# Performance work log

Measured on AMD Instinct MI355X. Metric: run time of the kernel, lower is better.

The kernel has to match this reference:

```python
import jax, jax.numpy as jnp
import numpy as np

B, N, DIM = 4, 2048, 128
K = 32            # num_nearest_neighbors
FF = 4            # fourier_features
M_DIM = 16
EDGE_IN = FF * 2 + DIM * 2 + 1  # 265


def setup_inputs() -> dict:
    key = jax.random.key(0)
    ks = jax.random.split(key, 16)
    std = 0.001  # init_eps normal init for Linear weights
    p = {
        "feats": jax.random.normal(ks[0], (B, N, DIM), jnp.float32),
        "coors": jax.random.normal(ks[1], (B, N, 3), jnp.float32),
        # edge_mlp: Linear(265, 530) -> SiLU -> Linear(530, 16) -> SiLU
        "eW1": jax.random.normal(ks[2], (EDGE_IN, EDGE_IN * 2), jnp.float32) * std,
        "eb1": jax.random.normal(ks[3], (EDGE_IN * 2,), jnp.float32) * std,
        "eW2": jax.random.normal(ks[4], (EDGE_IN * 2, M_DIM), jnp.float32) * std,
        "eb2": jax.random.normal(ks[5], (M_DIM,), jnp.float32) * std,
        # coors_mlp: Linear(16, 64) -> SiLU -> Linear(64, 1)
        "cW1": jax.random.normal(ks[6], (M_DIM, M_DIM * 4), jnp.float32) * std,
        "cb1": jax.random.normal(ks[7], (M_DIM * 4,), jnp.float32) * std,
        "cW2": jax.random.normal(ks[8], (M_DIM * 4, 1), jnp.float32) * std,
        "cb2": jax.random.normal(ks[9], (1,), jnp.float32) * std,
        # node_mlp: Linear(144, 256) -> SiLU -> Linear(256, 128)
        "nW1": jax.random.normal(ks[10], (DIM + M_DIM, DIM * 2), jnp.float32) * std,
        "nb1": jax.random.normal(ks[11], (DIM * 2,), jnp.float32) * std,
        "nW2": jax.random.normal(ks[12], (DIM * 2, DIM), jnp.float32) * std,
        "nb2": jax.random.normal(ks[13], (DIM,), jnp.float32) * std,
    }
    return p


def _egnn_fwd(feats, coors, eW1, eb1, eW2, eb2, cW1, cb1, cW2, cb2, nW1, nb1, nW2, nb2):
    # all-pairs squared distances: [b, n, n]
    rel_coors_full = coors[:, :, None, :] - coors[:, None, :, :]
    rel_dist = jnp.sum(rel_coors_full * rel_coors_full, axis=-1)

    # top-k nearest (smallest distance) -> indices [b, n, k]
    _, idx = jax.lax.top_k(-rel_dist, K)

    # gather neighbor coords / feats per batch: [b, n, k, *]
    coors_j = jax.vmap(lambda x, i: x[i])(coors, idx)
    feats_j = jax.vmap(lambda x, i: x[i])(feats, idx)
    rel_coors = coors[:, :, None, :] - coors_j                     # b n k 3
    d = jnp.take_along_axis(rel_dist, idx, axis=2)[..., None]       # b n k 1

    # fourier encode distances: [b, n, k, 2*FF + 1]
    scales = 2.0 ** jnp.arange(FF, dtype=feats.dtype)               # [FF]
    xs = d[..., None] / scales                                      # b n k 1 FF
    enc = jnp.concatenate([jnp.sin(xs), jnp.cos(xs), d[..., None]], axis=-1)
    enc = enc[..., 0, :]                                            # b n k (2FF+1)

    feats_i = jnp.broadcast_to(feats[:, :, None, :], feats_j.shape)
    edge_input = jnp.concatenate([feats_i, feats_j, enc], axis=-1)  # b n k 265

    # edge MLP -> messages m_ij [b, n, k, m_dim]
    h = jax.nn.silu(edge_input @ eW1 + eb1)
    m_ij = jax.nn.silu(h @ eW2 + eb2)

    # coors MLP -> per-edge coordinate weights [b, n, k]
    cw = (jax.nn.silu(m_ij @ cW1 + cb1) @ cW2 + cb2)[..., 0]
    coors_out = jnp.einsum('bij,bijc->bic', cw, rel_coors) + coors

    # node update: sum-pool messages, concat with feats, MLP + residual
    m_i = jnp.sum(m_ij, axis=-2)                                    # b n m_dim
    node_in = jnp.concatenate([feats, m_i], axis=-1)
    node_out = jax.nn.silu(node_in @ nW1 + nb1) @ nW2 + nb2 + feats
    return node_out, coors_out


def reference(feats, coors, eW1, eb1, eW2, eb2, cW1, cb1, cW2, cb2, nW1, nb1, nW2, nb2):
    return _egnn_fwd(feats, coors, eW1, eb1, eW2, eb2, cW1, cb1, cW2, cb2, nW1, nb1, nW2, nb2)
```

## Files before the change

### kernel.cpp

```cpp
#include <hip/hip_runtime.h>
#include <hip/hip_bf16.h>
#include <math.h>

#define Bb 4
#define Nn 2048
#define DIMd 128
#define Kk 32
#define H1 530
#define PW2 530
#define MD 16
#define NDH 256
#define NDI 144

typedef float f32x2 __attribute__((ext_vector_type(2)));
typedef float f32x4 __attribute__((ext_vector_type(4)));
typedef short s16x4 __attribute__((ext_vector_type(4)));
typedef short s16x8 __attribute__((ext_vector_type(8)));

__device__ __forceinline__ unsigned short f2bf(float f){
    union { float f; unsigned u; } v; v.f = f;
    unsigned r = v.u + 0x7FFFu + ((v.u >> 16) & 1u);
    return (unsigned short)(r >> 16);
}
__device__ __forceinline__ float silu_f(float x){
    float e = __builtin_amdgcn_exp2f(x * -1.442695041f);
    return x * __builtin_amdgcn_rcpf(1.0f + e);
}
__device__ __forceinline__ f32x2 silu2(f32x2 x){
    float e0 = __builtin_amdgcn_exp2f(x[0] * -1.442695041f);
    float e1 = __builtin_amdgcn_exp2f(x[1] * -1.442695041f);
    f32x2 r;
    r[0] = x[0] * __builtin_amdgcn_rcpf(1.0f + e0);
    r[1] = x[1] * __builtin_amdgcn_rcpf(1.0f + e1);
    return r;
}
__device__ __forceinline__ unsigned cvt_pk_bf16(float a, float b){
    unsigned r;
    asm("v_cvt_pk_bf16_f32 %0, %1, %2" : "=v"(r) : "v"(a), "v"(b));
    return r;
}

__global__ __launch_bounds__(256) void topk_kernel(const float* __restrict__ coors,
        int* __restrict__ idx_ws, float* __restrict__ dv_ws){
    int tid = threadIdx.x;
    int w = tid >> 6, lane = tid & 63;
    int node = blockIdx.x * 4 + w;
    int b = node >> 11;
    const float* cbp = coors + (size_t)b * Nn * 3;
    float cx = coors[node*3+0], cy = coors[node*3+1], cz = coors[node*3+2];
    float d[32];
    #pragma unroll
    for (int t = 0; t < 32; t++){
        int j = t*64 + lane;
        float dx = cx - cbp[j*3+0], dy = cy - cbp[j*3+1], dz = cz - cbp[j*3+2];
        d[t] = dx*dx + dy*dy + dz*dz;
    }
    float md = d[0]; int mj = lane;
    #pragma unroll
    for (int t = 1; t < 32; t++){
        int jt = t*64 + lane;
        if (d[t] < md){ md = d[t]; mj = jt; }
    }
    for (int r = 0; r < Kk; r++){
        float bd = md; int bj = mj;
        #pragma unroll
        for (int off = 32; off; off >>= 1){
            float d2 = __shfl_xor(bd, off); int j2 = __shfl_xor(bj, off);
            if (d2 < bd || (d2 == bd && j2 < bj)){ bd = d2; bj = j2; }
        }
        if (lane == 0){
            idx_ws[node*Kk + r] = bj;
            dv_ws[node*Kk + r] = bd;
        }
        if (mj == bj){
            md = 3.4e38f; mj = 0x7fffffff;
            #pragma unroll
            for (int t = 0; t < 32; t++){
                int jt = t*64 + lane;
                if (jt == bj) d[t] = 3.4e38f;
                if (d[t] < md){ md = d[t]; mj = jt; }
            }
        }
    }
}

__global__ __launch_bounds__(256) void fragw_kernel(const float* __restrict__ eW1,
        const float* __restrict__ eW2,
        unsigned short* __restrict__ W1F, unsigned short* __restrict__ WPF,
        unsigned short* __restrict__ W2F2){
    int i0 = blockIdx.x * 256 + threadIdx.x;
    int stride = gridDim.x * 256;
    for (int i = i0; i < 34*5*512; i += stride){
        int j = i & 7, lane = (i >> 3) & 63, t = i >> 9;
        int ks = t % 5, nt = t / 5;
        int cg = nt*16 + (lane & 15);
        int k = ks*32 + ((lane >> 4) << 3) + j;
        float v = 0.f;
        if (cg < H1){
            if (k < 128) v = eW1[(size_t)(128+k)*H1 + cg];
            else if (k < 137) v = eW1[(size_t)(256+(k-128))*H1 + cg];
        }
        W1F[i] = f2bf(v);
    }
    for (int i = i0; i < 34*4*512; i += stride){
        int j = i & 7, lane = (i >> 3) & 63, t = i >> 9;
        int ks = t & 3, nt = t >> 2;
        int cg = nt*16 + (lane & 15);
        int k = ks*32 + ((lane >> 4) << 3) + j;
        float v = (cg < H1) ? eW1[(size_t)k*H1 + cg] : 0.f;
        WPF[i] = f2bf(v);
    }
    for (int i = i0; i < 34*512; i += stride){
        int j = i & 7, lane = (i >> 3) & 63, nt = i >> 9;
        int kl = ((lane >> 4) << 3) + j;
        int col = lane & 15;
        int row = nt*16 + kl;
        float v = (kl < 16 && row < H1) ? eW2[(size_t)row*MD + col] : 0.f;
        W2F2[i] = f2bf(v);
    }
}

__global__ __launch_bounds__(256) void pmat_kernel(const float* __restrict__ feats,
        const unsigned short* __restrict__ WPF, const float* __restrict__ eb1,
        float* __restrict__ P){
    int tid = threadIdx.x;
    int wid = tid >> 6, lane = tid & 63;
    int node0 = blockIdx.x * 32;
    int kg = (lane >> 4) * 8;
    s16x8 af[2][4];
    #pragma unroll
    for (int m = 0; m < 2; m++){
        const float* fr = feats + (size_t)(node0 + m*16 + (lane & 15)) * DIMd;
        #pragma unroll
        for (int ks = 0; ks < 4; ks++){
            f32x4 lo = *(const f32x4*)(fr + ks*32 + kg);
            f32x4 hi = *(const f32x4*)(fr + ks*32 + kg + 4);
            union { s16x8 v; unsigned u[4]; } pk;
            pk.u[0] = cvt_pk_bf16(lo[0], lo[1]); pk.u[1] = cvt_pk_bf16(lo[2], lo[3]);
            pk.u[2] = cvt_pk_bf16(hi[0], hi[1]); pk.u[3] = cvt_pk_bf16(hi[2], hi[3]);
            af[m][ks] = pk.v;
        }
    }
    const s16x8* WPFv = (const s16x8*)WPF;
    for (int nt = wid; nt < 34; nt += 4){
        f32x4 acc0 = {0,0,0,0}, acc1 = {0,0,0,0};
        #pragma unroll
        for (int ks = 0; ks < 4; ks++){
            s16x8 bb = WPFv[(nt*4 + ks)*64 + lane];
            acc0 = __builtin_amdgcn_mfma_f32_16x16x32_bf16(af[0][ks], bb, acc0, 0, 0, 0);
            acc1 = __builtin_amdgcn_mfma_f32_16x16x32_bf16(af[1][ks], bb, acc1, 0, 0, 0);
        }
        int cg = nt*16 + (lane & 15);
        if (cg < H1){
            float b = eb1[cg];
            int r0 = (lane >> 4) * 4;
            #pragma unroll
            for (int r = 0; r < 4; r++){
                P[(size_t)(node0 + r0 + r)*PW2 + cg]      = acc0[r] + b;
                P[(size_t)(node0 + 16 + r0 + r)*PW2 + cg] = acc1[r] + b;
            }
        }
    }
}

#define TS 24
__global__ __launch_bounds__(256, 5) void edge_kernel(const float* __restrict__ coors,
        const float* __restrict__ feats, const float* __restrict__ eb2,
        const float* __restrict__ cW1, const float* __restrict__ cb1,
        const float* __restrict__ cW2, const float* __restrict__ cb2,
        const float* __restrict__ P, const unsigned short* __restrict__ W1F,
        const unsigned short* __restrict__ W2F2,
        const int* __restrict__ idx_ws, const float* __restrict__ dv_ws,
        float* __restrict__ mi_ws, float* __restrict__ coors_out){
    __shared__ float Pi_lds[544];
    __shared__ __align__(16) unsigned short aenc[Kk][32];
    __shared__ int js[Kk];
    __shared__ float rels[Kk][3];
    __shared__ unsigned short T[4][16][TS];
    __shared__ float m_red[4][Kk][MD];
    __shared__ float cacc[4][3];

    int node = blockIdx.x; int tid = threadIdx.x;
    int b = node >> 11;
    int wid = tid >> 6, lane = tid & 63;

    for (int t = tid; t < 4*16*(TS-16); t += 256){
        int w = t / (16*(TS-16)), rem = t % (16*(TS-16));
        T[w][rem / (TS-16)][16 + rem % (TS-16)] = 0;
    }
    const float* Pn = P + (size_t)node*PW2;
    Pi_lds[tid]       = Pn[tid];
    { int c = tid + 256; Pi_lds[c] = (c < PW2) ? Pn[c] : 0.f; }
    if (tid < 32){ int c = 512 + tid; Pi_lds[c] = (c < PW2) ? Pn[c] : 0.f; }
    if (tid < Kk){
        int j = idx_ws[node*Kk + tid];
        float dv = dv_ws[node*Kk + tid];
        js[tid] = j;
        unsigned short e[9];
        e[0] = f2bf(sinf(dv));        e[1] = f2bf(sinf(dv*0.5f));
        e[2] = f2bf(sinf(dv*0.25f));  e[3] = f2bf(sinf(dv*0.125f));
        e[4] = f2bf(cosf(dv));        e[5] = f2bf(cosf(dv*0.5f));
        e[6] = f2bf(cosf(dv*0.25f));  e[7] = f2bf(cosf(dv*0.125f));
        e[8] = f2bf(dv);
        #pragma unroll
        for (int q = 0; q < 9; q++) aenc[tid][q] = e[q];
        #pragma unroll
        for (int q = 9; q < 32; q++) aenc[tid][q] = 0;
        int jg = (b << 11) + j;
        rels[tid][0] = coors[node*3+0] - coors[jg*3+0];
        rels[tid][1] = coors[node*3+1] - coors[jg*3+1];
        rels[tid][2] = coors[node*3+2] - coors[jg*3+2];
    }
    __syncthreads();

    int kg = (lane >> 4) * 8;
    int kga = (kg >= 16) ? 16 : kg;
    s16x8 af[2][5];
    #pragma unroll
    for (int m = 0; m < 2; m++){
        int row = m*16 + (lane & 15);
        int jgl = (b << 11) + js[row];
        const float* fr = feats + (size_t)jgl * DIMd;
        #pragma unroll
        for (int ks = 0; ks < 4; ks++){
            f32x4 lo = *(const f32x4*)(fr + ks*32 + kg);
            f32x4 hi = *(const f32x4*)(fr + ks*32 + kg + 4);
            union { s16x8 v; unsigned u[4]; } pk;
            pk.u[0] = cvt_pk_bf16(lo[0], lo[1]); pk.u[1] = cvt_pk_bf16(lo[2], lo[3]);
            pk.u[2] = cvt_pk_bf16(hi[0], hi[1]); pk.u[3] = cvt_pk_bf16(hi[2], hi[3]);
            af[m][ks] = pk.v;
        }
        af[m][4] = *(const s16x8*)(&aenc[row][kg]);
    }

    const s16x8* W1Fv  = (const s16x8*)W1F;
    const s16x8* W2F2v = (const s16x8*)W2F2;
    f32x4 macc0 = {0,0,0,0}, macc1 = {0,0,0,0};
    int col = lane & 15, r0 = (lane >> 4) * 4;
    for (int nt = wid; nt < 34; nt += 4){
        f32x4 acc0 = {0,0,0,0}, acc1 = {0,0,0,0};
        #pragma unroll
        for (int ks = 0; ks < 5; ks++){
            s16x8 bb = W1Fv[(nt*5 + ks)*64 + lane];
            acc0 = __builtin_amdgcn_mfma_f32_16x16x32_bf16(af[0][ks], bb, acc0, 0, 0, 0);
            acc1 = __builtin_amdgcn_mfma_f32_16x16x32_bf16(af[1][ks], bb, acc1, 0, 0, 0);
        }
        int cg = nt*16 + col;
        bool valid = cg < H1;
        float pic = Pi_lds[cg];
        s16x8 w2b = W2F2v[nt*64 + lane];
        #pragma unroll
        for (int r = 0; r < 4; r++)
            T[wid][r0 + r][col] = valid ? f2bf(silu_f(acc0[r] + pic)) : (unsigned short)0;
        {
            union { s16x8 v; s16x4 h[2]; } a2;
            a2.h[0] = *(const s16x4*)&T[wid][col][kga];
            a2.h[1] = *(const s16x4*)&T[wid][col][kga + 4];
            macc0 = __builtin_amdgcn_mfma_f32_16x16x32_bf16(a2.v, w2b, macc0, 0, 0, 0);
        }
        #pragma unroll
        for (int r = 0; r < 4; r++)
            T[wid][r0 + r][col] = valid ? f2bf(silu_f(acc1[r] + pic)) : (unsigned short)0;
        {
            union { s16x8 v; s16x4 h[2]; } a2;
            a2.h[0] = *(const s16x4*)&T[wid][col][kga];
            a2.h[1] = *(const s16x4*)&T[wid][col][kga + 4];
            macc1 = __builtin_amdgcn_mfma_f32_16x16x32_bf16(a2.v, w2b, macc1, 0, 0, 0);
        }
    }
    #pragma unroll
    for (int r = 0; r < 4; r++){
        m_red[wid][r0 + r][col]      = macc0[r];
        m_red[wid][16 + r0 + r][col] = macc1[r];
    }
    __syncthreads();
    #pragma unroll
    for (int t = tid; t < Kk*MD; t += 256){
        int n = t >> 4, f = t & 15;
        float s = m_red[0][n][f] + m_red[1][n][f] + m_red[2][n][f] + m_red[3][n][f];
        m_red[0][n][f] = silu_f(s + eb2[f]);
    }
    __syncthreads();
    if (tid < MD){
        float s = 0.f;
        #pragma unroll
        for (int n = 0; n < Kk; n++) s += m_red[0][n][tid];
        mi_ws[node*MD + tid] = s;
    }
    float vx = 0.f, vy = 0.f, vz = 0.f;
    int u4 = col * 4;
    f32x4 cb14 = *(const f32x4*)(cb1 + u4);
    f32x4 c24  = *(const f32x4*)(cW2 + u4);
    #pragma unroll
    for (int q = 0; q < 2; q++){
        int eid = wid*8 + (lane >> 4)*2 + q;
        f32x4 acc4 = cb14;
        #pragma unroll
        for (int f = 0; f < MD; f++){
            float mv = m_red[0][eid][f];
            f32x4 w4 = *(const f32x4*)(cW1 + f*64 + u4);
            acc4 += (f32x4){mv,mv,mv,mv} * w4;
        }
        float p = silu_f(acc4[0])*c24[0] + silu_f(acc4[1])*c24[1]
                + silu_f(acc4[2])*c24[2] + silu_f(acc4[3])*c24[3];
        #pragma unroll
        for (int off = 1; off < 16; off <<= 1) p += __shfl_xor(p, off);
        float cw = p + cb2[0];
        if (col == 0){
            vx += cw * rels[eid][0];
            vy += cw * rels[eid][1];
            vz += cw * rels[eid][2];
        }
    }
    vx += __shfl_xor(vx, 16); vx += __shfl_xor(vx, 32);
    vy += __shfl_xor(vy, 16); vy += __shfl_xor(vy, 32);
    vz += __shfl_xor(vz, 16); vz += __shfl_xor(vz, 32);
    if (lane == 0){ cacc[wid][0] = vx; cacc[wid][1] = vy; cacc[wid][2] = vz; }
    __syncthreads();
    if (tid == 0){
        coors_out[node*3+0] = cacc[0][0]+cacc[1][0]+cacc[2][0]+cacc[3][0] + coors[node*3+0];
        coors_out[node*3+1] = cacc[0][1]+cacc[1][1]+cacc[2][1]+cacc[3][1] + coors[node*3+1];
        coors_out[node*3+2] = cacc[0][2]+cacc[1][2]+cacc[2][2]+cacc[3][2] + coors[node*3+2];
    }
}

__global__ __launch_bounds__(256) void node_kernel(const float* __restrict__ feats,
        const float* __restrict__ mi_ws,
        const float* __restrict__ nW1, const float* __restrict__ nb1,
        const float* __restrict__ nW2, const float* __restrict__ nb2,
        float* __restrict__ out){
    __shared__ float insT[NDI][12];
    __shared__ float hsdT[NDH][12];
    int tid = threadIdx.x;
    int node0 = blockIdx.x * 8;
    for (int t = tid; t < 8*DIMd; t += 256){
        int m = t >> 7, k = t & 127;
        insT[k][m] = feats[(size_t)node0*DIMd + t];
    }
    if (tid < 8*MD) insT[DIMd + (tid & 15)][tid >> 4] = mi_ws[node0*MD + tid];
    __syncthreads();
    float bias = nb1[tid];
    f32x2 acc[4];
    #pragma unroll
    for (int p = 0; p < 4; p++) acc[p] = (f32x2){bias, bias};
    for (int k = 0; k < NDI; k++){
        float wv = nW1[(size_t)k*NDH + tid];
        f32x2 w2 = {wv, wv};
        acc[0] += *(const f32x2*)&insT[k][0] * w2;
        acc[1] += *(const f32x2*)&insT[k][2] * w2;
        acc[2] += *(const f32x2*)&insT[k][4] * w2;
        acc[3] += *(const f32x2*)&insT[k][6] * w2;
    }
    #pragma unroll
    for (int p = 0; p < 4; p++) *(f32x2*)&hsdT[tid][2*p] = silu2(acc[p]);
    __syncthreads();
    int c = tid & 127, half = tid >> 7;
    float b2 = nb2[c];
    f32x2 a0 = {b2, b2}, a1 = {b2, b2};
    for (int k = 0; k < NDH; k++){
        float wv = nW2[(size_t)k*DIMd + c];
        f32x2 w2 = {wv, wv};
        a0 += *(const f32x2*)&hsdT[k][half*4]     * w2;
        a1 += *(const f32x2*)&hsdT[k][half*4 + 2] * w2;
    }
    #pragma unroll
    for (int q = 0; q < 4; q++){
        int m = half*4 + q;
        float v = (q < 2) ? a0[q & 1] : a1[q & 1];
        out[(size_t)(node0+m)*DIMd + c] = v + feats[(size_t)(node0+m)*DIMd + c];
    }
}

extern "C" void kernel_launch(void* const* d_in, const int* in_sizes, int n_in,
                              void* d_out, int out_size, void* d_ws, size_t ws_size,
                              hipStream_t stream){
    const float* feats = (const float*)d_in[0];
    const float* coors = (const float*)d_in[1];
    const float* eW1 = (const float*)d_in[2];
    const float* eb1 = (const float*)d_in[3];
    const float* eW2 = (const float*)d_in[4];
    const float* eb2 = (const float*)d_in[5];
    const float* cW1 = (const float*)d_in[6];
    const float* cb1 = (const float*)d_in[7];
    const float* cW2 = (const float*)d_in[8];
    const float* cb2 = (const float*)d_in[9];
    const float* nW1 = (const float*)d_in[10];
    const float* nb1 = (const float*)d_in[11];
    const float* nW2 = (const float*)d_in[12];
    const float* nb2 = (const float*)d_in[13];
    float* out = (float*)d_out;
    float* coors_out = out + (size_t)Bb*Nn*DIMd;

    char* ws = (char*)d_ws;
    size_t off = 0;
    int*   idx_ws = (int*)(ws + off);   off += (1u<<20);
    float* dv_ws  = (float*)(ws + off); off += (1u<<20);
    float* Pd     = (float*)(ws + off); off += 17367040u;
    float* mi_ws  = (float*)(ws + off); off += 524288u;
    unsigned short* W1F  = (unsigned short*)(ws + off); off += 174080u;
    unsigned short* WPF  = (unsigned short*)(ws + off); off += 139264u;
    unsigned short* W2F2 = (unsigned short*)(ws + off); off += 34816u;

    fragw_kernel<<<256, 256, 0, stream>>>(eW1, eW2, W1F, WPF, W2F2);
    pmat_kernel<<<Bb*Nn/32, 256, 0, stream>>>(feats, WPF, eb1, Pd);
    topk_kernel<<<Bb*Nn/4, 256, 0, stream>>>(coors, idx_ws, dv_ws);
    edge_kernel<<<Bb*Nn, 256, 0, stream>>>(coors, feats, eb2, cW1, cb1, cW2, cb2,
                                           Pd, W1F, W2F2, idx_ws, dv_ws, mi_ws, coors_out);
    node_kernel<<<Bb*Nn/8, 256, 0, stream>>>(feats, mi_ws, nW1, nb1, nW2, nb2, out);
}
```

Baseline: 304.9 us.

## Merge topk and pmat kernels; transpose edge MFMAs, pass hidden via bpermute

Merges the top-k and P-matrix kernels into one launch that branches on block index, so both independent stages can run concurrently and one launch is saved. In the edge kernel it swaps the MFMA operand order, putting weights in the A operand and edge features in B. The silu'd hidden tile then stays in registers and is redistributed with ds_bpermute for the second MFMA, replacing the per-wave LDS transpose buffer and its zero-fill. It also pads m_red against bank conflicts and raises the occupancy hint from 5 to 8 waves, which risks register spills.

```diff
diff --git a/kernel.cpp b/kernel.cpp
--- a/kernel.cpp
+++ b/kernel.cpp
@@ -11,10 +11,11 @@
 #define MD 16
 #define NDH 256
 #define NDI 144
+#define TOPK_BLKS (Bb*Nn/4)
+#define PMAT_BLKS (Bb*Nn/32)
 
 typedef float f32x2 __attribute__((ext_vector_type(2)));
 typedef float f32x4 __attribute__((ext_vector_type(4)));
-typedef short s16x4 __attribute__((ext_vector_type(4)));
 typedef short s16x8 __attribute__((ext_vector_type(8)));
 
 __device__ __forceinline__ unsigned short f2bf(float f){
@@ -38,50 +39,6 @@
     unsigned r;
     asm("v_cvt_pk_bf16_f32 %0, %1, %2" : "=v"(r) : "v"(a), "v"(b));
     return r;
-}
-
-__global__ __launch_bounds__(256) void topk_kernel(const float* __restrict__ coors,
-        int* __restrict__ idx_ws, float* __restrict__ dv_ws){
-    int tid = threadIdx.x;
-    int w = tid >> 6, lane = tid & 63;
-    int node = blockIdx.x * 4 + w;
-    int b = node >> 11;
-    const float* cbp = coors + (size_t)b * Nn * 3;
-    float cx = coors[node*3+0], cy = coors[node*3+1], cz = coors[node*3+2];
-    float d[32];
-    #pragma unroll
-    for (int t = 0; t < 32; t++){
-        int j = t*64 + lane;
-        float dx = cx - cbp[j*3+0], dy = cy - cbp[j*3+1], dz = cz - cbp[j*3+2];
-        d[t] = dx*dx + dy*dy + dz*dz;
-    }
-    float md = d[0]; int mj = lane;
-    #pragma unroll
-    for (int t = 1; t < 32; t++){
-        int jt = t*64 + lane;
-        if (d[t] < md){ md = d[t]; mj = jt; }
-    }
-    for (int r = 0; r < Kk; r++){
-        float bd = md; int bj = mj;
-        #pragma unroll
-        for (int off = 32; off; off >>= 1){
-            float d2 = __shfl_xor(bd, off); int j2 = __shfl_xor(bj, off);
-            if (d2 < bd || (d2 == bd && j2 < bj)){ bd = d2; bj = j2; }
-        }
-        if (lane == 0){
-            idx_ws[node*Kk + r] = bj;
-            dv_ws[node*Kk + r] = bd;
-        }
-        if (mj == bj){
-            md = 3.4e38f; mj = 0x7fffffff;
-            #pragma unroll
-            for (int t = 0; t < 32; t++){
-                int jt = t*64 + lane;
-                if (jt == bj) d[t] = 3.4e38f;
-                if (d[t] < md){ md = d[t]; mj = jt; }
-            }
-        }
-    }
 }
 
 __global__ __launch_bounds__(256) void fragw_kernel(const float* __restrict__ eW1,
@@ -120,51 +77,94 @@
     }
 }
 
-__global__ __launch_bounds__(256) void pmat_kernel(const float* __restrict__ feats,
+__global__ __launch_bounds__(256) void prep_kernel(const float* __restrict__ coors,
+        const float* __restrict__ feats,
         const unsigned short* __restrict__ WPF, const float* __restrict__ eb1,
-        float* __restrict__ P){
+        int* __restrict__ idx_ws, float* __restrict__ dv_ws, float* __restrict__ P){
+    int bid = blockIdx.x;
     int tid = threadIdx.x;
-    int wid = tid >> 6, lane = tid & 63;
-    int node0 = blockIdx.x * 32;
-    int kg = (lane >> 4) * 8;
-    s16x8 af[2][4];
-    #pragma unroll
-    for (int m = 0; m < 2; m++){
-        const float* fr = feats + (size_t)(node0 + m*16 + (lane & 15)) * DIMd;
-        #pragma unroll
-        for (int ks = 0; ks < 4; ks++){
-            f32x4 lo = *(const f32x4*)(fr + ks*32 + kg);
-            f32x4 hi = *(const f32x4*)(fr + ks*32 + kg + 4);
-            union { s16x8 v; unsigned u[4]; } pk;
-            pk.u[0] = cvt_pk_bf16(lo[0], lo[1]); pk.u[1] = cvt_pk_bf16(lo[2], lo[3]);
-            pk.u[2] = cvt_pk_bf16(hi[0], hi[1]); pk.u[3] = cvt_pk_bf16(hi[2], hi[3]);
-            af[m][ks] = pk.v;
-        }
-    }
-    const s16x8* WPFv = (const s16x8*)WPF;
-    for (int nt = wid; nt < 34; nt += 4){
-        f32x4 acc0 = {0,0,0,0}, acc1 = {0,0,0,0};
-        #pragma unroll
-        for (int ks = 0; ks < 4; ks++){
-            s16x8 bb = WPFv[(nt*4 + ks)*64 + lane];
-            acc0 = __builtin_amdgcn_mfma_f32_16x16x32_bf16(af[0][ks], bb, acc0, 0, 0, 0);
-            acc1 = __builtin_amdgcn_mfma_f32_16x16x32_bf16(af[1][ks], bb, acc1, 0, 0, 0);
-        }
-        int cg = nt*16 + (lane & 15);
-        if (cg < H1){
-            float b = eb1[cg];
-            int r0 = (lane >> 4) * 4;
+    if (bid < TOPK_BLKS){
+        int w = tid >> 6, lane = tid & 63;
+        int node = bid * 4 + w;
+        int b = node >> 11;
+        const float* cbp = coors + (size_t)b * Nn * 3;
+        float cx = coors[node*3+0], cy = coors[node*3+1], cz = coors[node*3+2];
+        float d[32];
+        #pragma unroll
+        for (int t = 0; t < 32; t++){
+            int j = t*64 + lane;
+            float dx = cx - cbp[j*3+0], dy = cy - cbp[j*3+1], dz = cz - cbp[j*3+2];
+            d[t] = dx*dx + dy*dy + dz*dz;
+        }
+        float md = d[0]; int mj = lane;
+        #pragma unroll
+        for (int t = 1; t < 32; t++){
+            int jt = t*64 + lane;
+            if (d[t] < md){ md = d[t]; mj = jt; }
+        }
+        for (int r = 0; r < Kk; r++){
+            float bd = md; int bj = mj;
             #pragma unroll
-            for (int r = 0; r < 4; r++){
-                P[(size_t)(node0 + r0 + r)*PW2 + cg]      = acc0[r] + b;
-                P[(size_t)(node0 + 16 + r0 + r)*PW2 + cg] = acc1[r] + b;
-            }
-        }
-    }
-}
-
-#define TS 24
-__global__ __launch_bounds__(256, 5) void edge_kernel(const float* __restrict__ coors,
+            for (int off = 32; off; off >>= 1){
+                float d2 = __shfl_xor(bd, off); int j2 = __shfl_xor(bj, off);
+                if (d2 < bd || (d2 == bd && j2 < bj)){ bd = d2; bj = j2; }
+            }
+            if (lane == 0){
+                idx_ws[node*Kk + r] = bj;
+                dv_ws[node*Kk + r] = bd;
+            }
+            if (mj == bj){
+                md = 3.4e38f; mj = 0x7fffffff;
+                #pragma unroll
+                for (int t = 0; t < 32; t++){
+                    int jt = t*64 + lane;
+                    if (jt == bj) d[t] = 3.4e38f;
+                    if (d[t] < md){ md = d[t]; mj = jt; }
+                }
+            }
+        }
+    } else {
+        int wid = tid >> 6, lane = tid & 63;
+        int node0 = (bid - TOPK_BLKS) * 32;
+        int kg = (lane >> 4) * 8;
+        s16x8 af[2][4];
+        #pragma unroll
+        for (int m = 0; m < 2; m++){
+            const float* fr = feats + (size_t)(node0 + m*16 + (lane & 15)) * DIMd;
+            #pragma unroll
+            for (int ks = 0; ks < 4; ks++){
+                f32x4 lo = *(const f32x4*)(fr + ks*32 + kg);
+                f32x4 hi = *(const f32x4*)(fr + ks*32 + kg + 4);
+                union { s16x8 v; unsigned u[4]; } pk;
+                pk.u[0] = cvt_pk_bf16(lo[0], lo[1]); pk.u[1] = cvt_pk_bf16(lo[2], lo[3]);
+                pk.u[2] = cvt_pk_bf16(hi[0], hi[1]); pk.u[3] = cvt_pk_bf16(hi[2], hi[3]);
+                af[m][ks] = pk.v;
+            }
+        }
+        const s16x8* WPFv = (const s16x8*)WPF;
+        for (int nt = wid; nt < 34; nt += 4){
+            f32x4 acc0 = {0,0,0,0}, acc1 = {0,0,0,0};
+            #pragma unroll
+            for (int ks = 0; ks < 4; ks++){
+                s16x8 bb = WPFv[(nt*4 + ks)*64 + lane];
+                acc0 = __builtin_amdgcn_mfma_f32_16x16x32_bf16(af[0][ks], bb, acc0, 0, 0, 0);
+                acc1 = __builtin_amdgcn_mfma_f32_16x16x32_bf16(af[1][ks], bb, acc1, 0, 0, 0);
+            }
+            int cg = nt*16 + (lane & 15);
+            if (cg < H1){
+                float b = eb1[cg];
+                int r0 = (lane >> 4) * 4;
+                #pragma unroll
+                for (int r = 0; r < 4; r++){
+                    P[(size_t)(node0 + r0 + r)*PW2 + cg]      = acc0[r] + b;
+                    P[(size_t)(node0 + 16 + r0 + r)*PW2 + cg] = acc1[r] + b;
+                }
+            }
+        }
+    }
+}
+
+__global__ __launch_bounds__(256, 8) void edge_kernel(const float* __restrict__ coors,
         const float* __restrict__ feats, const float* __restrict__ eb2,
         const float* __restrict__ cW1, const float* __restrict__ cb1,
         const float* __restrict__ cW2, const float* __restrict__ cb2,
@@ -176,18 +176,13 @@
     __shared__ __align__(16) unsigned short aenc[Kk][32];
     __shared__ int js[Kk];
     __shared__ float rels[Kk][3];
-    __shared__ unsigned short T[4][16][TS];
-    __shared__ float m_red[4][Kk][MD];
+    __shared__ float m_red[4][Kk][MD+1];
     __shared__ float cacc[4][3];
 
     int node = blockIdx.x; int tid = threadIdx.x;
     int b = node >> 11;
     int wid = tid >> 6, lane = tid & 63;
 
-    for (int t = tid; t < 4*16*(TS-16); t += 256){
-        int w = t / (16*(TS-16)), rem = t % (16*(TS-16));
-        T[w][rem / (TS-16)][16 + rem % (TS-16)] = 0;
-    }
     const float* Pn = P + (size_t)node*PW2;
     Pi_lds[tid]       = Pn[tid];
     { int c = tid + 256; Pi_lds[c] = (c < PW2) ? Pn[c] : 0.f; }
@@ -214,11 +209,11 @@
     __syncthreads();
 
     int kg = (lane >> 4) * 8;
-    int kga = (kg >= 16) ? 16 : kg;
+    int grp = lane >> 4, n16 = lane & 15;
     s16x8 af[2][5];
     #pragma unroll
     for (int m = 0; m < 2; m++){
-        int row = m*16 + (lane & 15);
+        int row = m*16 + n16;
         int jgl = (b << 11) + js[row];
         const float* fr = feats + (size_t)jgl * DIMd;
         #pragma unroll
@@ -233,45 +228,49 @@
         af[m][4] = *(const s16x8*)(&aenc[row][kg]);
     }
 
+    int addr1 = ((((2*grp)    ) << 4) | n16) << 2;
+    int addr2 = ((((2*grp) + 1) << 4) | n16) << 2;
+
     const s16x8* W1Fv  = (const s16x8*)W1F;
     const s16x8* W2F2v = (const s16x8*)W2F2;
     f32x4 macc0 = {0,0,0,0}, macc1 = {0,0,0,0};
-    int col = lane & 15, r0 = (lane >> 4) * 4;
     for (int nt = wid; nt < 34; nt += 4){
         f32x4 acc0 = {0,0,0,0}, acc1 = {0,0,0,0};
         #pragma unroll
         for (int ks = 0; ks < 5; ks++){
-            s16x8 bb = W1Fv[(nt*5 + ks)*64 + lane];
-            acc0 = __builtin_amdgcn_mfma_f32_16x16x32_bf16(af[0][ks], bb, acc0, 0, 0, 0);
-            acc1 = __builtin_amdgcn_mfma_f32_16x16x32_bf16(af[1][ks], bb, acc1, 0, 0, 0);
-        }
-        int cg = nt*16 + col;
-        bool valid = cg < H1;
-        float pic = Pi_lds[cg];
-        s16x8 w2b = W2F2v[nt*64 + lane];
-        #pragma unroll
-        for (int r = 0; r < 4; r++)
-            T[wid][r0 + r][col] = valid ? f2bf(silu_f(acc0[r] + pic)) : (unsigned short)0;
-        {
-            union { s16x8 v; s16x4 h[2]; } a2;
-            a2.h[0] = *(const s16x4*)&T[wid][col][kga];
-            a2.h[1] = *(const s16x4*)&T[wid][col][kga + 4];
-            macc0 = __builtin_amdgcn_mfma_f32_16x16x32_bf16(a2.v, w2b, macc0, 0, 0, 0);
-        }
-        #pragma unroll
-        for (int r = 0; r < 4; r++)
-            T[wid][r0 + r][col] = valid ? f2bf(silu_f(acc1[r] + pic)) : (unsigned short)0;
-        {
-            union { s16x8 v; s16x4 h[2]; } a2;
-            a2.h[0] = *(const s16x4*)&T[wid][col][kga];
-            a2.h[1] = *(const s16x4*)&T[wid][col][kga + 4];
-            macc1 = __builtin_amdgcn_mfma_f32_16x16x32_bf16(a2.v, w2b, macc1, 0, 0, 0);
-        }
+            s16x8 aw = W1Fv[(nt*5 + ks)*64 + lane];
+            acc0 = __builtin_amdgcn_mfma_f32_16x16x32_bf16(aw, af[0][ks], acc0, 0, 0, 0);
+            acc1 = __builtin_amdgcn_mfma_f32_16x16x32_bf16(aw, af[1][ks], acc1, 0, 0, 0);
+        }
+        s16x8 w2a = W2F2v[nt*64 + lane];
+        int cgb = nt*16 + grp*4;
+        float x0[4], x1[4];
+        #pragma unroll
+        for (int r = 0; r < 4; r++){
+            int cg = cgb + r;
+            bool valid = cg < H1;
+            float pic = Pi_lds[cg];
+            x0[r] = valid ? silu_f(acc0[r] + pic) : 0.f;
+            x1[r] = valid ? silu_f(acc1[r] + pic) : 0.f;
+        }
+        unsigned p00 = cvt_pk_bf16(x0[0], x0[1]), p01 = cvt_pk_bf16(x0[2], x0[3]);
+        unsigned p10 = cvt_pk_bf16(x1[0], x1[1]), p11 = cvt_pk_bf16(x1[2], x1[3]);
+        union { s16x8 v; int u[4]; } b0, b1;
+        b0.u[0] = __builtin_amdgcn_ds_bpermute(addr1, (int)p00);
+        b0.u[1] = __builtin_amdgcn_ds_bpermute(addr1, (int)p01);
+        b0.u[2] = __builtin_amdgcn_ds_bpermute(addr2, (int)p00);
+        b0.u[3] = __builtin_amdgcn_ds_bpermute(addr2, (int)p01);
+        b1.u[0] = __builtin_amdgcn_ds_bpermute(addr1, (int)p10);
+        b1.u[1] = __builtin_amdgcn_ds_bpermute(addr1, (int)p11);
+        b1.u[2] = __builtin_amdgcn_ds_bpermute(addr2, (int)p10);
+        b1.u[3] = __builtin_amdgcn_ds_bpermute(addr2, (int)p11);
+        macc0 = __builtin_amdgcn_mfma_f32_16x16x32_bf16(w2a, b0.v, macc0, 0, 0, 0);
+        macc1 = __builtin_amdgcn_mfma_f32_16x16x32_bf16(w2a, b1.v, macc1, 0, 0, 0);
     }
     #pragma unroll
     for (int r = 0; r < 4; r++){
-        m_red[wid][r0 + r][col]      = macc0[r];
-        m_red[wid][16 + r0 + r][col] = macc1[r];
+        m_red[wid][n16][grp*4 + r]      = macc0[r];
+        m_red[wid][16 + n16][grp*4 + r] = macc1[r];
     }
     __syncthreads();
     #pragma unroll
@@ -288,12 +287,12 @@
         mi_ws[node*MD + tid] = s;
     }
     float vx = 0.f, vy = 0.f, vz = 0.f;
-    int u4 = col * 4;
+    int u4 = n16 * 4;
     f32x4 cb14 = *(const f32x4*)(cb1 + u4);
     f32x4 c24  = *(const f32x4*)(cW2 + u4);
     #pragma unroll
     for (int q = 0; q < 2; q++){
-        int eid = wid*8 + (lane >> 4)*2 + q;
+        int eid = wid*8 + grp*2 + q;
         f32x4 acc4 = cb14;
         #pragma unroll
         for (int f = 0; f < MD; f++){
@@ -306,7 +305,7 @@
         #pragma unroll
         for (int off = 1; off < 16; off <<= 1) p += __shfl_xor(p, off);
         float cw = p + cb2[0];
-        if (col == 0){
+        if (n16 == 0){
             vx += cw * rels[eid][0];
             vy += cw * rels[eid][1];
             vz += cw * rels[eid][2];
@@ -402,8 +401,8 @@
     unsigned short* W2F2 = (unsigned short*)(ws + off); off += 34816u;
 
     fragw_kernel<<<256, 256, 0, stream>>>(eW1, eW2, W1F, WPF, W2F2);
-    pmat_kernel<<<Bb*Nn/32, 256, 0, stream>>>(feats, WPF, eb1, Pd);
-    topk_kernel<<<Bb*Nn/4, 256, 0, stream>>>(coors, idx_ws, dv_ws);
+    prep_kernel<<<TOPK_BLKS + PMAT_BLKS, 256, 0, stream>>>(coors, feats, WPF, eb1,
+                                                           idx_ws, dv_ws, Pd);
     edge_kernel<<<Bb*Nn, 256, 0, stream>>>(coors, feats, eb2, cW1, cb1, cW2, cb2,
                                            Pd, W1F, W2F2, idx_ws, dv_ws, mi_ws, coors_out);
     node_kernel<<<Bb*Nn/8, 256, 0, stream>>>(feats, mi_ws, nW1, nb1, nW2, nb2, out);
```

Result: slower. 421.7 us (+38.3%).
